# Optimization experiments

Hardware: AMD Instinct MI355X
Metric: run time of the kernel (lower is better)

Reference implementation:

```python
import jax, jax.numpy as jnp
import numpy as np

HIDDEN = 2048
NUM_HEADS = 16
HEAD_DIM = HIDDEN // NUM_HEADS
INTER = 8192
EPS = 1e-6


def setup_inputs() -> dict:
    key = jax.random.key(0)
    ks = jax.random.split(key, 10)
    s = 0.02
    return {
        "x": jax.random.normal(ks[0], (2, 2048, HIDDEN), dtype=jnp.float32),
        "w_ln1": jnp.ones((HIDDEN,), dtype=jnp.float32),
        "wq": jax.random.normal(ks[1], (HIDDEN, HIDDEN), dtype=jnp.float32) * s,
        "wk": jax.random.normal(ks[2], (HIDDEN, HIDDEN), dtype=jnp.float32) * s,
        "wv": jax.random.normal(ks[3], (HIDDEN, HIDDEN), dtype=jnp.float32) * s,
        "wo": jax.random.normal(ks[4], (HIDDEN, HIDDEN), dtype=jnp.float32) * s,
        "w_ln2": jnp.ones((HIDDEN,), dtype=jnp.float32),
        "wg": jax.random.normal(ks[5], (INTER, HIDDEN), dtype=jnp.float32) * s,
        "wu": jax.random.normal(ks[6], (INTER, HIDDEN), dtype=jnp.float32) * s,
        "wd": jax.random.normal(ks[7], (HIDDEN, INTER), dtype=jnp.float32) * s,
    }


def rmsnorm(x, w):
    rms = jnp.sqrt(jnp.mean(x * x, axis=-1, keepdims=True) + EPS)
    return x / rms * w


def attention(x, wq, wk, wv, wo):
    B, T, C = x.shape
    # weights are [out, in] (torch Linear convention) -> x @ W.T
    q = (x @ wq.T).reshape(B, T, NUM_HEADS, HEAD_DIM)
    k = (x @ wk.T).reshape(B, T, NUM_HEADS, HEAD_DIM)
    v = (x @ wv.T).reshape(B, T, NUM_HEADS, HEAD_DIM)
    scores = jnp.einsum("bqhd,bkhd->bhqk", q, k) / jnp.sqrt(jnp.float32(HEAD_DIM))
    attn = jax.nn.softmax(scores, axis=-1)
    out = jnp.einsum("bhqk,bkhd->bqhd", attn, v).reshape(B, T, C)
    return out @ wo.T


def mlp(x, wg, wu, wd):
    return (jax.nn.silu(x @ wg.T) * (x @ wu.T)) @ wd.T


def reference(x, w_ln1, wq, wk, wv, wo, w_ln2, wg, wu, wd):
    x = x + attention(rmsnorm(x, w_ln1), wq, wk, wv, wo)
    x = x + mlp(rmsnorm(x, w_ln2), wg, wu, wd)
    return x
```

## Files before the change

kernel.cpp:

```cpp
#include <hip/hip_runtime.h>
#include <stdint.h>

typedef unsigned short u16;
typedef unsigned int   u32;
typedef short s16x8 __attribute__((ext_vector_type(8)));
typedef u16   u16x8 __attribute__((ext_vector_type(8)));
typedef u32   u32x4 __attribute__((ext_vector_type(4)));
typedef float f32x4 __attribute__((ext_vector_type(4)));

__device__ __forceinline__ u16 f2bf(float f) {
    u32 u = __float_as_uint(f);
    u32 r = u + 0x7fffu + ((u >> 16) & 1u);
    return (u16)(r >> 16);
}
__device__ __forceinline__ float bf2f(u16 h) {
    return __uint_as_float(((u32)h) << 16);
}

__device__ __forceinline__ u32 cvtpk(float a, float b) {
    u32 r;
    asm("v_cvt_pk_bf16_f32 %0, %1, %2" : "=v"(r) : "v"(a), "v"(b));
    return r;
}
__device__ __forceinline__ void swap32(u32& a, u32& b) {
#if __has_builtin(__builtin_amdgcn_permlane32_swap)
    auto r = __builtin_amdgcn_permlane32_swap(a, b, false, false);
    a = r[0]; b = r[1];
#else
    asm volatile("v_permlane32_swap_b32 %0, %1" : "+v"(a), "+v"(b));
#endif
}
__device__ __forceinline__ void swap16(u32& a, u32& b) {
#if __has_builtin(__builtin_amdgcn_permlane16_swap)
    auto r = __builtin_amdgcn_permlane16_swap(a, b, false, false);
    a = r[0]; b = r[1];
#else
    asm volatile("v_permlane16_swap_b32 %0, %1" : "+v"(a), "+v"(b));
#endif
}

#define GLD16(gp, lp) __builtin_amdgcn_global_load_lds(                          \
    (const __attribute__((address_space(1))) void*)(uintptr_t)(gp),             \
    (__attribute__((address_space(3))) void*)(u32)(uintptr_t)(lp), 16, 0, 0)

#define FENCE asm volatile("" ::: "memory")

template<int N> __device__ __forceinline__ void waitv() {
    if constexpr (N == 0)      asm volatile("s_waitcnt vmcnt(0)" ::: "memory");
    else if constexpr (N == 3) asm volatile("s_waitcnt vmcnt(3)" ::: "memory");
    else                       asm volatile("s_waitcnt vmcnt(4)" ::: "memory");
}

__global__ __launch_bounds__(256)
void cast_w(const float* __restrict__ in, u16* __restrict__ out, int n)
{
    const int i = (blockIdx.x * 256 + threadIdx.x) * 8;
    if (i >= n) return;
    f32x4 a = *(const f32x4*)(in + i);
    f32x4 b = *(const f32x4*)(in + i + 4);
    u16x8 o;
    o[0] = f2bf(a[0]); o[1] = f2bf(a[1]); o[2] = f2bf(a[2]); o[3] = f2bf(a[3]);
    o[4] = f2bf(b[0]); o[5] = f2bf(b[1]); o[6] = f2bf(b[2]); o[7] = f2bf(b[3]);
    *(u16x8*)(out + i) = o;
}

__global__ __launch_bounds__(256)
void rmsnorm_k(const float* __restrict__ x, const float* __restrict__ wln,
               u16* __restrict__ out, int C)
{
    const int row = blockIdx.x;
    const int tid = threadIdx.x;
    const float* xr = x + (size_t)row * C;
    f32x4 a = *(const f32x4*)(xr + tid * 8);
    f32x4 b = *(const f32x4*)(xr + tid * 8 + 4);
    float s = a[0]*a[0] + a[1]*a[1] + a[2]*a[2] + a[3]*a[3]
            + b[0]*b[0] + b[1]*b[1] + b[2]*b[2] + b[3]*b[3];
    #pragma unroll
    for (int off = 1; off < 64; off <<= 1) s += __shfl_xor(s, off);
    __shared__ float red[4];
    if ((tid & 63) == 0) red[tid >> 6] = s;
    __syncthreads();
    float tot = red[0] + red[1] + red[2] + red[3];
    float inv = rsqrtf(tot / (float)C + 1e-6f);
    f32x4 wa = *(const f32x4*)(wln + tid * 8);
    f32x4 wb = *(const f32x4*)(wln + tid * 8 + 4);
    u16x8 o;
    o[0] = f2bf(a[0]*inv*wa[0]); o[1] = f2bf(a[1]*inv*wa[1]);
    o[2] = f2bf(a[2]*inv*wa[2]); o[3] = f2bf(a[3]*inv*wa[3]);
    o[4] = f2bf(b[0]*inv*wb[0]); o[5] = f2bf(b[1]*inv*wb[1]);
    o[6] = f2bf(b[2]*inv*wb[2]); o[7] = f2bf(b[3]*inv*wb[3]);
    *(u16x8*)(out + (size_t)row * C + tid * 8) = o;
}

template<int MODE, int MR>
__global__ __launch_bounds__(512, 1)
void gemm8(const u16* __restrict__ A, const u16* __restrict__ W,
           const float* __restrict__ resid, const u16* __restrict__ aux,
           void* __restrict__ Cout, int M, int N, int K, float scale)
{
    constexpr int BM  = MR * 32;
    constexpr int MR2 = MR / 2;
    constexpr int SRA = MR * 8;
    constexpr int AL  = BM / 128;
    constexpr int WS  = 2 + AL;
    __shared__ __align__(16) u16 lds[2][(BM + 256) * 64];

    const int tid  = threadIdx.x;
    const int lane = tid & 63;
    const int w    = tid >> 6;
    const int wm   = w >> 2;
    const int wn   = w & 3;

    const int gx  = N >> 8;
    const int nwg = gridDim.x;
    const int sid = ((int)blockIdx.x & 7) * (nwg >> 3) + ((int)blockIdx.x >> 3);
    const int brow = (sid / gx) * BM;
    const int bcol = (sid % gx) * 256;

    const int KT = K >> 6;
    const int NI = KT >> 1;

    f32x4 acc[MR][4] = {};

    auto stageA = [&](int buf, int g, int kt) {
        #pragma unroll
        for (int j = 0; j < AL; ++j) {
            const int p   = j * 64 + (tid >> 3);
            const int row = ((p & ~(SRA - 1)) << 1) | (g * SRA) | (p & (SRA - 1));
            const int ch  = (tid & 7) ^ (row & 7);
            const u16* src = A + (size_t)(brow + row) * K + kt * 64 + ch * 8;
            const int p0  = j * 64 + (w << 3);
            const int r0  = ((p0 & ~(SRA - 1)) << 1) | (g * SRA) | (p0 & (SRA - 1));
            GLD16(src, &lds[buf][0] + r0 * 64);
        }
    };
    auto stageB = [&](int buf, int g, int kt) {
        #pragma unroll
        for (int j = 0; j < 2; ++j) {
            const int p   = j * 64 + (tid >> 3);
            const int row = ((p & ~31) << 1) | (g * 32) | (p & 31);
            const int ch  = (tid & 7) ^ (row & 7);
            const u16* src = W + (size_t)(bcol + row) * K + kt * 64 + ch * 8;
            const int p0  = j * 64 + (w << 3);
            const int r0  = ((p0 & ~31) << 1) | (g * 32) | (p0 & 31);
            GLD16(src, &lds[buf][BM * 64] + r0 * 64);
        }
    };

#define LDA(AF, MH, Ab)                                                          \
    _Pragma("unroll") for (int f = 0; f < MR2; ++f)                              \
    _Pragma("unroll") for (int ks = 0; ks < 2; ++ks) {                           \
        const int row = wm * (BM / 2) + (MH) * (BM / 4) + f * 16 + (lane & 15);  \
        const int ch  = (ks * 4 + (lane >> 4)) ^ (row & 7);                      \
        AF[f][ks] = *(const s16x8*)((Ab) + row * 64 + ch * 8);                   \
    }
#define LDB(BQ, NH, Bb)                                                          \
    _Pragma("unroll") for (int g = 0; g < 2; ++g)                                \
    _Pragma("unroll") for (int ks = 0; ks < 2; ++ks) {                           \
        const int row = wn * 64 + (NH) * 32 + g * 16 + (lane & 15);              \
        const int ch  = (ks * 4 + (lane >> 4)) ^ (row & 7);                      \
        BQ[g][ks] = *(const s16x8*)((Bb) + row * 64 + ch * 8);                   \
    }
#define MFQ(AF, BQ, MH, NH)                                                      \
    __builtin_amdgcn_s_setprio(1);                                               \
    _Pragma("unroll") for (int f = 0; f < MR2; ++f)                              \
    _Pragma("unroll") for (int g = 0; g < 2; ++g)                                \
    _Pragma("unroll") for (int ks = 0; ks < 2; ++ks)                             \
        acc[(MH) * MR2 + f][(NH) * 2 + g] =                                      \
            __builtin_amdgcn_mfma_f32_16x16x32_bf16(                             \
                AF[f][ks], BQ[g][ks], acc[(MH) * MR2 + f][(NH) * 2 + g], 0, 0, 0); \
    __builtin_amdgcn_s_setprio(0);
#define BAR1 FENCE; __builtin_amdgcn_s_barrier(); FENCE
#define ENDP asm volatile("s_waitcnt lgkmcnt(0)" ::: "memory");                  \
             FENCE; __builtin_amdgcn_s_barrier(); FENCE

#define KTILE(BUF, S1, S2, S3, S4, W4)                                           \
    {                                                                            \
        const u16* Ab = &lds[BUF][0];                                            \
        const u16* Bb = &lds[BUF][BM * 64];                                      \
        s16x8 afq[MR2][2], bq0[2][2], bq1[2][2];                                 \
        LDA(afq, 0, Ab) LDB(bq0, 0, Bb)                                          \
        S1; BAR1; MFQ(afq, bq0, 0, 0) ENDP;                                      \
        LDB(bq1, 1, Bb)                                                          \
        S2; BAR1; MFQ(afq, bq1, 0, 1) ENDP;                                      \
        LDA(afq, 1, Ab)                                                          \
        S3; BAR1; MFQ(afq, bq1, 1, 1) ENDP;                                      \
        S4; W4; BAR1; MFQ(afq, bq0, 1, 0) ENDP;                                  \
    }

    stageB(0, 0, 0); stageA(0, 1, 0); stageA(0, 0, 0); stageB(0, 1, 0);
    stageB(1, 0, 1); stageA(1, 1, 1);
    waitv<WS>();
    FENCE; __builtin_amdgcn_s_barrier(); FENCE;

    for (int it = 0; it < NI; ++it) {
        const int t1  = 2 * it + 1;
        const int t0n = 2 * it + 2;
        const int t1n = 2 * it + 3;
        const bool s0 = t0n < KT, s1 = t1n < KT;
        const bool last = (it == NI - 1);

        KTILE(0,
              { stageB(1, 1, t1); },
              { stageA(1, 0, t1); },
              { if (s0) stageB(0, 0, t0n); },
              { if (s0) stageA(0, 1, t0n); },
              { if (last) waitv<0>(); else waitv<WS>(); })
        KTILE(1,
              { if (s0) stageA(0, 0, t0n); },
              { if (s0) stageB(0, 1, t0n); },
              { if (s1) stageB(1, 0, t1n); },
              { if (s1) stageA(1, 1, t1n); },
              { if (!last) waitv<WS>(); })
    }
#undef KTILE
#undef LDA
#undef LDB
#undef MFQ
#undef BAR1
#undef ENDP

    const int er = (lane >> 4) * 4;
    const int ec = lane & 15;
    #pragma unroll
    for (int i = 0; i < MR; ++i) {
        #pragma unroll
        for (int j = 0; j < 4; ++j) {
            #pragma unroll
            for (int r = 0; r < 4; ++r) {
                const int row = brow + wm * (BM / 2) + i * 16 + er + r;
                const int col = bcol + wn * 64 + j * 16 + ec;
                const size_t idx = (size_t)row * N + col;
                const float va = acc[i][j][r];
                if (MODE == 0)      ((u16*)Cout)[idx] = f2bf(va);
                else if (MODE == 1) ((u16*)Cout)[idx] = f2bf(va * scale);
                else if (MODE == 2) ((float*)Cout)[idx] = resid[idx] + va;
                else {
                    const float g  = bf2f(aux[idx]);
                    const float sg = g / (1.0f + exp2f(-g * 1.4426950408889634f));
                    ((u16*)Cout)[idx] = f2bf(sg * va);
                }
            }
        }
    }
}

__global__ __launch_bounds__(512, 2)
void flash_attn(const u16* __restrict__ q, const u16* __restrict__ k,
                const u16* __restrict__ vT, u16* __restrict__ o)
{
    __shared__ __align__(16) u16 Kt[2][64 * 128];
    __shared__ __align__(16) u16 Vt[2][128 * 64];
    const int tid  = threadIdx.x;
    const int lane = tid & 63;
    const int w    = tid >> 6;
    const int qtile = blockIdx.x;
    const int bh    = blockIdx.y;
    const int b = bh >> 4, h = bh & 15;
    const size_t head  = ((size_t)b * 2048) * 2048 + (size_t)h * 128;
    const size_t vbase = ((size_t)h * 128) * 4096 + (size_t)b * 2048;

    s16x8 qf[2][4];
    #pragma unroll
    for (int qi = 0; qi < 2; ++qi) {
        const int tq = qtile * 256 + w * 32 + qi * 16 + (lane & 15);
        const u16* qp = q + head + (size_t)tq * 2048 + (lane >> 4) * 8;
        #pragma unroll
        for (int dk = 0; dk < 4; ++dk) qf[qi][dk] = *(const s16x8*)(qp + dk * 32);
    }

    f32x4 oa[2][8] = {};
    float m_r[2] = {-1e30f, -1e30f};
    float l_r[2] = {0.f, 0.f};

    const int krow = tid >> 3;
    const int kcol = (tid & 7) * 16;
    const int vd   = tid >> 2;
    const int vk   = (tid & 3) * 16;
    const u16* kg = k + head + (size_t)krow * 2048 + kcol;
    const u16* vg = vT + vbase + (size_t)vd * 4096 + vk;
    const u32 kw0 = (u32)((krow * 256 + kcol * 2)      ^ ((krow & 7) << 4));
    const u32 kw1 = (u32)((krow * 256 + kcol * 2 + 16) ^ ((krow & 7) << 4));
    const u32 vw0 = (u32)((vd * 128 + vk * 2)          ^ ((vd & 7) << 4));
    const u32 vw1 = (u32)((vd * 128 + vk * 2 + 16)     ^ ((vd & 7) << 4));

    s16x8 kr0 = *(const s16x8*)(kg);
    s16x8 kr1 = *(const s16x8*)(kg + 8);
    s16x8 vr0 = *(const s16x8*)(vg);
    s16x8 vr1 = *(const s16x8*)(vg + 8);

    for (int kb = 0; kb < 32; ++kb) {
        const int cur = kb & 1;
        char* KtB = (char*)&Kt[cur][0];
        char* VtB = (char*)&Vt[cur][0];
        *(s16x8*)(KtB + kw0) = kr0;
        *(s16x8*)(KtB + kw1) = kr1;
        *(s16x8*)(VtB + vw0) = vr0;
        *(s16x8*)(VtB + vw1) = vr1;
        if (kb + 1 < 32) {
            const int k0n = (kb + 1) * 64;
            kr0 = *(const s16x8*)(kg + (size_t)k0n * 2048);
            kr1 = *(const s16x8*)(kg + (size_t)k0n * 2048 + 8);
            vr0 = *(const s16x8*)(vg + k0n);
            vr1 = *(const s16x8*)(vg + k0n + 8);
        }
        asm volatile("s_waitcnt lgkmcnt(0)" ::: "memory");
        __builtin_amdgcn_s_barrier();
        FENCE;

        f32x4 st[2][4] = {};
        __builtin_amdgcn_s_setprio(1);
        #pragma unroll
        for (int kt = 0; kt < 4; ++kt) {
            const int row = kt * 16 + (lane & 15);
            s16x8 kf[4];
            #pragma unroll
            for (int dk = 0; dk < 4; ++dk) {
                const int dcol = dk * 32 + (lane >> 4) * 8;
                kf[dk] = *(const s16x8*)(KtB + ((row * 256 + dcol * 2) ^ ((row & 7) << 4)));
            }
            #pragma unroll
            for (int qi = 0; qi < 2; ++qi)
                #pragma unroll
                for (int dk = 0; dk < 4; ++dk)
                    st[qi][kt] = __builtin_amdgcn_mfma_f32_16x16x32_bf16(kf[dk], qf[qi][dk], st[qi][kt], 0, 0, 0);
        }
        __builtin_amdgcn_s_setprio(0);

        float mx[2];
        #pragma unroll
        for (int qi = 0; qi < 2; ++qi) {
            float m0 = fmaxf(fmaxf(st[qi][0][0], st[qi][0][1]), fmaxf(st[qi][0][2], st[qi][0][3]));
            float m1 = fmaxf(fmaxf(st[qi][1][0], st[qi][1][1]), fmaxf(st[qi][1][2], st[qi][1][3]));
            float m2 = fmaxf(fmaxf(st[qi][2][0], st[qi][2][1]), fmaxf(st[qi][2][2], st[qi][2][3]));
            float m3 = fmaxf(fmaxf(st[qi][3][0], st[qi][3][1]), fmaxf(st[qi][3][2], st[qi][3][3]));
            float m0123 = fmaxf(fmaxf(m0, m1), fmaxf(m2, m3));
            m0123 = fmaxf(m0123, __shfl_xor(m0123, 16));
            m0123 = fmaxf(m0123, __shfl_xor(m0123, 32));
            mx[qi] = m0123;
        }
        const bool grow = (mx[0] > m_r[0] + 8.f) || (mx[1] > m_r[1] + 8.f);
        if (__any(grow)) {
            #pragma unroll
            for (int qi = 0; qi < 2; ++qi) {
                const float mn = fmaxf(m_r[qi], mx[qi]);
                const float sc = exp2f(m_r[qi] - mn);
                m_r[qi] = mn;
                l_r[qi] *= sc;
                const float s0 = __shfl(sc, (lane >> 4) * 4 + 0);
                const float s1 = __shfl(sc, (lane >> 4) * 4 + 1);
                const float s2 = __shfl(sc, (lane >> 4) * 4 + 2);
                const float s3 = __shfl(sc, (lane >> 4) * 4 + 3);
                #pragma unroll
                for (int ni = 0; ni < 8; ++ni) {
                    oa[qi][ni][0] *= s0; oa[qi][ni][1] *= s1;
                    oa[qi][ni][2] *= s2; oa[qi][ni][3] *= s3;
                }
            }
        }

        s16x8 pa[2][2];
        #pragma unroll
        for (int qi = 0; qi < 2; ++qi) {
            float sum = 0.f;
            #pragma unroll
            for (int kt = 0; kt < 4; ++kt)
                #pragma unroll
                for (int r = 0; r < 4; ++r) {
                    const float p = exp2f(st[qi][kt][r] - m_r[qi]);
                    st[qi][kt][r] = p;
                    sum += p;
                }
            sum += __shfl_xor(sum, 16);
            sum += __shfl_xor(sum, 32);
            l_r[qi] += sum;

            u32 q01[4], q23[4];
            #pragma unroll
            for (int kt = 0; kt < 4; ++kt) {
                q01[kt] = cvtpk(st[qi][kt][0], st[qi][kt][1]);
                q23[kt] = cvtpk(st[qi][kt][2], st[qi][kt][3]);
            }
            #pragma unroll
            for (int ks = 0; ks < 2; ++ks) {
                u32 X = q01[2 * ks], Y = q01[2 * ks + 1];
                swap32(X, Y); swap16(X, Y);
                u32 U = q23[2 * ks], V = q23[2 * ks + 1];
                swap32(U, V); swap16(U, V);
                u32x4 t; t[0] = X; t[1] = U; t[2] = Y; t[3] = V;
                pa[qi][ks] = __builtin_bit_cast(s16x8, t);
            }
        }

        __builtin_amdgcn_s_setprio(1);
        #pragma unroll
        for (int ks = 0; ks < 2; ++ks) {
            const int keyb = ks * 32 + (lane >> 4) * 8;
            #pragma unroll
            for (int ni = 0; ni < 8; ++ni) {
                const int dd = ni * 16 + (lane & 15);
                s16x8 vf = *(const s16x8*)(VtB + ((dd * 128 + keyb * 2) ^ ((dd & 7) << 4)));
                #pragma unroll
                for (int qi = 0; qi < 2; ++qi)
                    oa[qi][ni] = __builtin_amdgcn_mfma_f32_16x16x32_bf16(pa[qi][ks], vf, oa[qi][ni], 0, 0, 0);
            }
        }
        __builtin_amdgcn_s_setprio(0);
    }
    #pragma unroll
    for (int qi = 0; qi < 2; ++qi) {
        #pragma unroll
        for (int r = 0; r < 4; ++r) {
            const float inv = 1.0f / __shfl(l_r[qi], (lane >> 4) * 4 + r);
            const int tout = qtile * 256 + w * 32 + qi * 16 + (lane >> 4) * 4 + r;
            u16* op = o + head + (size_t)tout * 2048 + (lane & 15);
            #pragma unroll
            for (int ni = 0; ni < 8; ++ni)
                op[ni * 16] = f2bf(oa[qi][ni][r] * inv);
        }
    }
}

extern "C" void kernel_launch(void* const* d_in, const int* in_sizes, int n_in,
                              void* d_out, int out_size, void* d_ws, size_t ws_size,
                              hipStream_t stream)
{
    (void)in_sizes; (void)n_in; (void)out_size; (void)ws_size;
    const float* x    = (const float*)d_in[0];
    const float* wln1 = (const float*)d_in[1];
    const float* wq   = (const float*)d_in[2];
    const float* wk   = (const float*)d_in[3];
    const float* wv   = (const float*)d_in[4];
    const float* wo   = (const float*)d_in[5];
    const float* wln2 = (const float*)d_in[6];
    const float* wg   = (const float*)d_in[7];
    const float* wu   = (const float*)d_in[8];
    const float* wd   = (const float*)d_in[9];
    float* out = (float*)d_out;

    const size_t MB = 1024ull * 1024ull;
    char* ws = (char*)d_ws;
    u16*   arena = (u16*)(ws + 0);
    float* hbuf  = (float*)(ws + 32 * MB);
    u16*   xn    = (u16*)(ws + 64 * MB);
    u16*   qb    = (u16*)(ws + 80 * MB);
    u16*   kbuf  = (u16*)(ws + 96 * MB);
    u16*   vT    = (u16*)(ws + 112 * MB);
    u16*   abuf  = (u16*)(ws + 128 * MB);
    u16*   gbuf  = (u16*)(ws + 80 * MB);

    const int M = 4096, C = 2048, I = 8192;
    const float qscale = 0.1275164899f;
    dim3 blk(256);
    dim3 blk8(512);

    rmsnorm_k<<<M, blk, 0, stream>>>(x, wln1, xn, C);

    cast_w<<<(C * C) / 2048, blk, 0, stream>>>(wq, arena, C * C);
    gemm8<1, 4><<<dim3((C / 256) * (M / 128)), blk8, 0, stream>>>(xn, arena, nullptr, nullptr, qb, M, C, C, qscale);
    cast_w<<<(C * C) / 2048, blk, 0, stream>>>(wk, arena, C * C);
    gemm8<0, 4><<<dim3((C / 256) * (M / 128)), blk8, 0, stream>>>(xn, arena, nullptr, nullptr, kbuf, M, C, C, 1.f);
    cast_w<<<(C * C) / 2048, blk, 0, stream>>>(wv, arena, C * C);
    gemm8<0, 4><<<dim3((M / 256) * (C / 128)), blk8, 0, stream>>>(arena, xn, nullptr, nullptr, vT, C, M, C, 1.f);

    flash_attn<<<dim3(2048 / 256, 32), blk8, 0, stream>>>(qb, kbuf, vT, abuf);

    cast_w<<<(C * C) / 2048, blk, 0, stream>>>(wo, arena, C * C);
    gemm8<2, 4><<<dim3((C / 256) * (M / 128)), blk8, 0, stream>>>(abuf, arena, x, nullptr, hbuf, M, C, C, 1.f);

    rmsnorm_k<<<M, blk, 0, stream>>>(hbuf, wln2, xn, C);

    cast_w<<<(I * C) / 2048, blk, 0, stream>>>(wg, arena, I * C);
    gemm8<0, 8><<<dim3((I / 256) * (M / 256)), blk8, 0, stream>>>(xn, arena, nullptr, nullptr, gbuf, M, I, C, 1.f);
    cast_w<<<(I * C) / 2048, blk, 0, stream>>>(wu, arena, I * C);
    gemm8<3, 8><<<dim3((I / 256) * (M / 256)), blk8, 0, stream>>>(xn, arena, nullptr, gbuf, gbuf, M, I, C, 1.f);
    cast_w<<<(C * I) / 2048, blk, 0, stream>>>(wd, arena, C * I);
    gemm8<2, 4><<<dim3((C / 256) * (M / 128)), blk8, 0, stream>>>(gbuf, arena, hbuf, nullptr, out, M, C, I, 1.f);
}
```

Measured before the change: 718.9 us.

## Replace ping-pong quarter-tile GEMM with simple triple-buffered K loop

Result: slower. 812.5 us (+13.0%).

```diff
diff --git a/kernel.cpp b/kernel.cpp
--- a/kernel.cpp
+++ b/kernel.cpp
@@ -47,7 +47,7 @@
 
 template<int N> __device__ __forceinline__ void waitv() {
     if constexpr (N == 0)      asm volatile("s_waitcnt vmcnt(0)" ::: "memory");
-    else if constexpr (N == 3) asm volatile("s_waitcnt vmcnt(3)" ::: "memory");
+    else if constexpr (N == 6) asm volatile("s_waitcnt vmcnt(6)" ::: "memory");
     else                       asm volatile("s_waitcnt vmcnt(4)" ::: "memory");
 }
 
@@ -92,18 +92,14 @@
     *(u16x8*)(out + (size_t)row * C + tid * 8) = o;
 }
 
-template<int MODE, int MR>
+template<int MODE>
 __global__ __launch_bounds__(512, 1)
-void gemm8(const u16* __restrict__ A, const u16* __restrict__ W,
+void gemm3(const u16* __restrict__ A, const u16* __restrict__ W,
            const float* __restrict__ resid, const u16* __restrict__ aux,
            void* __restrict__ Cout, int M, int N, int K, float scale)
 {
-    constexpr int BM  = MR * 32;
-    constexpr int MR2 = MR / 2;
-    constexpr int SRA = MR * 8;
-    constexpr int AL  = BM / 128;
-    constexpr int WS  = 2 + AL;
-    __shared__ __align__(16) u16 lds[2][(BM + 256) * 64];
+    constexpr int BM = 128;
+    __shared__ __align__(16) u16 lds[3][(BM + 256) * 64];
 
     const int tid  = threadIdx.x;
     const int lane = tid & 63;
@@ -118,117 +114,84 @@
     const int bcol = (sid % gx) * 256;
 
     const int KT = K >> 6;
-    const int NI = KT >> 1;
-
-    f32x4 acc[MR][4] = {};
-
-    auto stageA = [&](int buf, int g, int kt) {
-        #pragma unroll
-        for (int j = 0; j < AL; ++j) {
-            const int p   = j * 64 + (tid >> 3);
-            const int row = ((p & ~(SRA - 1)) << 1) | (g * SRA) | (p & (SRA - 1));
+
+    f32x4 acc[4][4] = {};
+
+    auto stageTile = [&](int buf, int kt) {
+        #pragma unroll
+        for (int g = 0; g < 2; ++g) {
+            #pragma unroll
+            for (int j = 0; j < 2; ++j) {
+                const int p   = j * 64 + (tid >> 3);
+                const int row = ((p & ~31) << 1) | (g * 32) | (p & 31);
+                const int ch  = (tid & 7) ^ (row & 7);
+                const u16* src = W + (size_t)(bcol + row) * K + kt * 64 + ch * 8;
+                const int p0  = j * 64 + (w << 3);
+                const int r0  = ((p0 & ~31) << 1) | (g * 32) | (p0 & 31);
+                GLD16(src, &lds[buf][BM * 64] + r0 * 64);
+            }
+        }
+        #pragma unroll
+        for (int g = 0; g < 2; ++g) {
+            const int p   = tid >> 3;
+            const int row = ((p & ~31) << 1) | (g * 32) | (p & 31);
             const int ch  = (tid & 7) ^ (row & 7);
             const u16* src = A + (size_t)(brow + row) * K + kt * 64 + ch * 8;
-            const int p0  = j * 64 + (w << 3);
-            const int r0  = ((p0 & ~(SRA - 1)) << 1) | (g * SRA) | (p0 & (SRA - 1));
+            const int p0  = w << 3;
+            const int r0  = ((p0 & ~31) << 1) | (g * 32) | (p0 & 31);
             GLD16(src, &lds[buf][0] + r0 * 64);
         }
     };
-    auto stageB = [&](int buf, int g, int kt) {
-        #pragma unroll
-        for (int j = 0; j < 2; ++j) {
-            const int p   = j * 64 + (tid >> 3);
-            const int row = ((p & ~31) << 1) | (g * 32) | (p & 31);
-            const int ch  = (tid & 7) ^ (row & 7);
-            const u16* src = W + (size_t)(bcol + row) * K + kt * 64 + ch * 8;
-            const int p0  = j * 64 + (w << 3);
-            const int r0  = ((p0 & ~31) << 1) | (g * 32) | (p0 & 31);
-            GLD16(src, &lds[buf][BM * 64] + r0 * 64);
-        }
-    };
-
-#define LDA(AF, MH, Ab)                                                          \
-    _Pragma("unroll") for (int f = 0; f < MR2; ++f)                              \
-    _Pragma("unroll") for (int ks = 0; ks < 2; ++ks) {                           \
-        const int row = wm * (BM / 2) + (MH) * (BM / 4) + f * 16 + (lane & 15);  \
-        const int ch  = (ks * 4 + (lane >> 4)) ^ (row & 7);                      \
-        AF[f][ks] = *(const s16x8*)((Ab) + row * 64 + ch * 8);                   \
+
+    stageTile(0, 0);
+    stageTile(1, 1);
+
+    for (int t = 0; t < KT; ++t) {
+        const int cur = t % 3;
+        if (t == KT - 1) waitv<0>(); else waitv<6>();
+        FENCE; __builtin_amdgcn_s_barrier(); FENCE;
+        if (t + 2 < KT) stageTile((t + 2) % 3, t + 2);
+
+        const u16* Ab = &lds[cur][0];
+        const u16* Bb = &lds[cur][BM * 64];
+        s16x8 af[4][2], bf[4][2];
+        #pragma unroll
+        for (int i = 0; i < 4; ++i)
+            #pragma unroll
+            for (int ks = 0; ks < 2; ++ks) {
+                const int row = wm * 64 + i * 16 + (lane & 15);
+                const int ch  = (ks * 4 + (lane >> 4)) ^ (row & 7);
+                af[i][ks] = *(const s16x8*)(Ab + row * 64 + ch * 8);
+            }
+        #pragma unroll
+        for (int j = 0; j < 4; ++j)
+            #pragma unroll
+            for (int ks = 0; ks < 2; ++ks) {
+                const int row = wn * 64 + j * 16 + (lane & 15);
+                const int ch  = (ks * 4 + (lane >> 4)) ^ (row & 7);
+                bf[j][ks] = *(const s16x8*)(Bb + row * 64 + ch * 8);
+            }
+        __builtin_amdgcn_s_setprio(1);
+        #pragma unroll
+        for (int i = 0; i < 4; ++i)
+            #pragma unroll
+            for (int j = 0; j < 4; ++j)
+                #pragma unroll
+                for (int ks = 0; ks < 2; ++ks)
+                    acc[i][j] = __builtin_amdgcn_mfma_f32_16x16x32_bf16(
+                        af[i][ks], bf[j][ks], acc[i][j], 0, 0, 0);
+        __builtin_amdgcn_s_setprio(0);
     }
-#define LDB(BQ, NH, Bb)                                                          \
-    _Pragma("unroll") for (int g = 0; g < 2; ++g)                                \
-    _Pragma("unroll") for (int ks = 0; ks < 2; ++ks) {                           \
-        const int row = wn * 64 + (NH) * 32 + g * 16 + (lane & 15);              \
-        const int ch  = (ks * 4 + (lane >> 4)) ^ (row & 7);                      \
-        BQ[g][ks] = *(const s16x8*)((Bb) + row * 64 + ch * 8);                   \
-    }
-#define MFQ(AF, BQ, MH, NH)                                                      \
-    __builtin_amdgcn_s_setprio(1);                                               \
-    _Pragma("unroll") for (int f = 0; f < MR2; ++f)                              \
-    _Pragma("unroll") for (int g = 0; g < 2; ++g)                                \
-    _Pragma("unroll") for (int ks = 0; ks < 2; ++ks)                             \
-        acc[(MH) * MR2 + f][(NH) * 2 + g] =                                      \
-            __builtin_amdgcn_mfma_f32_16x16x32_bf16(                             \
-                AF[f][ks], BQ[g][ks], acc[(MH) * MR2 + f][(NH) * 2 + g], 0, 0, 0); \
-    __builtin_amdgcn_s_setprio(0);
-#define BAR1 FENCE; __builtin_amdgcn_s_barrier(); FENCE
-#define ENDP asm volatile("s_waitcnt lgkmcnt(0)" ::: "memory");                  \
-             FENCE; __builtin_amdgcn_s_barrier(); FENCE
-
-#define KTILE(BUF, S1, S2, S3, S4, W4)                                           \
-    {                                                                            \
-        const u16* Ab = &lds[BUF][0];                                            \
-        const u16* Bb = &lds[BUF][BM * 64];                                      \
-        s16x8 afq[MR2][2], bq0[2][2], bq1[2][2];                                 \
-        LDA(afq, 0, Ab) LDB(bq0, 0, Bb)                                          \
-        S1; BAR1; MFQ(afq, bq0, 0, 0) ENDP;                                      \
-        LDB(bq1, 1, Bb)                                                          \
-        S2; BAR1; MFQ(afq, bq1, 0, 1) ENDP;                                      \
-        LDA(afq, 1, Ab)                                                          \
-        S3; BAR1; MFQ(afq, bq1, 1, 1) ENDP;                                      \
-        S4; W4; BAR1; MFQ(afq, bq0, 1, 0) ENDP;                                  \
-    }
-
-    stageB(0, 0, 0); stageA(0, 1, 0); stageA(0, 0, 0); stageB(0, 1, 0);
-    stageB(1, 0, 1); stageA(1, 1, 1);
-    waitv<WS>();
-    FENCE; __builtin_amdgcn_s_barrier(); FENCE;
-
-    for (int it = 0; it < NI; ++it) {
-        const int t1  = 2 * it + 1;
-        const int t0n = 2 * it + 2;
-        const int t1n = 2 * it + 3;
-        const bool s0 = t0n < KT, s1 = t1n < KT;
-        const bool last = (it == NI - 1);
-
-        KTILE(0,
-              { stageB(1, 1, t1); },
-              { stageA(1, 0, t1); },
-              { if (s0) stageB(0, 0, t0n); },
-              { if (s0) stageA(0, 1, t0n); },
-              { if (last) waitv<0>(); else waitv<WS>(); })
-        KTILE(1,
-              { if (s0) stageA(0, 0, t0n); },
-              { if (s0) stageB(0, 1, t0n); },
-              { if (s1) stageB(1, 0, t1n); },
-              { if (s1) stageA(1, 1, t1n); },
-              { if (!last) waitv<WS>(); })
-    }
-#undef KTILE
-#undef LDA
-#undef LDB
-#undef MFQ
-#undef BAR1
-#undef ENDP
 
     const int er = (lane >> 4) * 4;
     const int ec = lane & 15;
     #pragma unroll
-    for (int i = 0; i < MR; ++i) {
+    for (int i = 0; i < 4; ++i) {
         #pragma unroll
         for (int j = 0; j < 4; ++j) {
             #pragma unroll
             for (int r = 0; r < 4; ++r) {
-                const int row = brow + wm * (BM / 2) + i * 16 + er + r;
+                const int row = brow + wm * 64 + i * 16 + er + r;
                 const int col = bcol + wn * 64 + j * 16 + ec;
                 const size_t idx = (size_t)row * N + col;
                 const float va = acc[i][j][r];
@@ -457,23 +420,23 @@
     rmsnorm_k<<<M, blk, 0, stream>>>(x, wln1, xn, C);
 
     cast_w<<<(C * C) / 2048, blk, 0, stream>>>(wq, arena, C * C);
-    gemm8<1, 4><<<dim3((C / 256) * (M / 128)), blk8, 0, stream>>>(xn, arena, nullptr, nullptr, qb, M, C, C, qscale);
+    gemm3<1><<<dim3((C / 256) * (M / 128)), blk8, 0, stream>>>(xn, arena, nullptr, nullptr, qb, M, C, C, qscale);
     cast_w<<<(C * C) / 2048, blk, 0, stream>>>(wk, arena, C * C);
-    gemm8<0, 4><<<dim3((C / 256) * (M / 128)), blk8, 0, stream>>>(xn, arena, nullptr, nullptr, kbuf, M, C, C, 1.f);
+    gemm3<0><<<dim3((C / 256) * (M / 128)), blk8, 0, stream>>>(xn, arena, nullptr, nullptr, kbuf, M, C, C, 1.f);
     cast_w<<<(C * C) / 2048, blk, 0, stream>>>(wv, arena, C * C);
-    gemm8<0, 4><<<dim3((M / 256) * (C / 128)), blk8, 0, stream>>>(arena, xn, nullptr, nullptr, vT, C, M, C, 1.f);
+    gemm3<0><<<dim3((M / 256) * (C / 128)), blk8, 0, stream>>>(arena, xn, nullptr, nullptr, vT, C, M, C, 1.f);
 
     flash_attn<<<dim3(2048 / 256, 32), blk8, 0, stream>>>(qb, kbuf, vT, abuf);
 
     cast_w<<<(C * C) / 2048, blk, 0, stream>>>(wo, arena, C * C);
-    gemm8<2, 4><<<dim3((C / 256) * (M / 128)), blk8, 0, stream>>>(abuf, arena, x, nullptr, hbuf, M, C, C, 1.f);
+    gemm3<2><<<dim3((C / 256) * (M / 128)), blk8, 0, stream>>>(abuf, arena, x, nullptr, hbuf, M, C, C, 1.f);
 
     rmsnorm_k<<<M, blk, 0, stream>>>(hbuf, wln2, xn, C);
 
     cast_w<<<(I * C) / 2048, blk, 0, stream>>>(wg, arena, I * C);
-    gemm8<0, 8><<<dim3((I / 256) * (M / 256)), blk8, 0, stream>>>(xn, arena, nullptr, nullptr, gbuf, M, I, C, 1.f);
+    gemm3<0><<<dim3((I / 256) * (M / 128)), blk8, 0, stream>>>(xn, arena, nullptr, nullptr, gbuf, M, I, C, 1.f);
     cast_w<<<(I * C) / 2048, blk, 0, stream>>>(wu, arena, I * C);
-    gemm8<3, 8><<<dim3((I / 256) * (M / 256)), blk8, 0, stream>>>(xn, arena, nullptr, gbuf, gbuf, M, I, C, 1.f);
+    gemm3<3><<<dim3((I / 256) * (M / 128)), blk8, 0, stream>>>(xn, arena, nullptr, gbuf, gbuf, M, I, C, 1.f);
     cast_w<<<(C * I) / 2048, blk, 0, stream>>>(wd, arena, C * I);
-    gemm8<2, 4><<<dim3((C / 256) * (M / 128)), blk8, 0, stream>>>(gbuf, arena, hbuf, nullptr, out, M, C, I, 1.f);
-}
+    gemm3<2><<<dim3((C / 256) * (M / 128)), blk8, 0, stream>>>(gbuf, arena, hbuf, nullptr, out, M, C, I, 1.f);
+}
```
